# Kernel tuning notes

Hardware: AMD Instinct MI355X
Metric: run time of the kernel (lower is better)

## Reference

```python
import jax, jax.numpy as jnp
import numpy as np

N_NODES = 100000
N_EDGES = 1600000
EMB = 128
EDGE_DIMS = [6, 3]
BN_EPS = 1e-5


def setup_inputs() -> dict:
    key = jax.random.key(0)
    ks = jax.random.split(key, 16)
    inp = {
        "node_feats": jax.random.normal(ks[0], (N_NODES, EMB), jnp.float32),
        "edge_feat_0": jax.random.uniform(ks[1], (N_EDGES, EDGE_DIMS[0]), jnp.float32),
        "edge_feat_1": jax.random.uniform(ks[2], (N_EDGES, EDGE_DIMS[1]), jnp.float32),
        "src": jax.random.randint(ks[3], (N_EDGES,), 0, N_NODES, jnp.int32),
        "dst": jax.random.randint(ks[4], (N_EDGES,), 0, N_NODES, jnp.int32),
    }
    # edge embedding linears (MLP num_layers==1 -> plain Linear)
    s0 = 1.0 / np.sqrt(EDGE_DIMS[0])
    s1 = 1.0 / np.sqrt(EDGE_DIMS[1])
    inp["We0"] = jax.random.uniform(ks[5], (EDGE_DIMS[0], EMB), jnp.float32, -s0, s0)
    inp["be0"] = jax.random.uniform(ks[6], (EMB,), jnp.float32, -s0, s0)
    inp["We1"] = jax.random.uniform(ks[7], (EDGE_DIMS[1], EMB), jnp.float32, -s1, s1)
    inp["be1"] = jax.random.uniform(ks[8], (EMB,), jnp.float32, -s1, s1)
    # mlp: Linear(emb, 2*emb) -> ReLU -> Linear(2*emb, emb)
    sm = 1.0 / np.sqrt(EMB)
    sh = 1.0 / np.sqrt(2 * EMB)
    inp["W1"] = jax.random.uniform(ks[9], (EMB, 2 * EMB), jnp.float32, -sm, sm)
    inp["b1"] = jax.random.uniform(ks[10], (2 * EMB,), jnp.float32, -sm, sm)
    inp["W2"] = jax.random.uniform(ks[11], (2 * EMB, EMB), jnp.float32, -sh, sh)
    inp["b2"] = jax.random.uniform(ks[12], (EMB,), jnp.float32, -sh, sh)
    # batch norm affine params
    inp["gamma"] = jnp.ones((EMB,), jnp.float32)
    inp["beta"] = jnp.zeros((EMB,), jnp.float32)
    return inp


def reference(node_feats, edge_feat_0, edge_feat_1, src, dst,
              We0, be0, We1, be1, W1, b1, W2, b2, gamma, beta):
    n_nodes = node_feats.shape[0]
    # per-family edge embeddings, summed
    edge_embs = (edge_feat_0 @ We0 + be0) + (edge_feat_1 @ We1 + be1)  # [E, D]
    # u_add_e: gather src node feats, add edge emb
    msgs = node_feats[src] + edge_embs  # [E, D]
    # scatter-sum to destination nodes
    agg = jax.ops.segment_sum(msgs, dst, num_segments=n_nodes)  # [N, D]
    # MLP: Linear -> ReLU -> Linear
    h = jax.nn.relu(agg @ W1 + b1) @ W2 + b2  # [N, D]
    # BatchNorm1d (training mode: batch statistics, biased variance)
    mean = jnp.mean(h, axis=0)
    var = jnp.var(h, axis=0)
    h = (h - mean) * jax.lax.rsqrt(var + BN_EPS) * gamma + beta
    return h
```

## Files before the change

kernel.cpp:

```cpp
#include <hip/hip_runtime.h>

#define N_NODES 100000
#define N_EDGES 1600000
#define EMB 128
#define BM 16
#define NSLAB 64
#define BN_EPS 1e-5f

#define SCAN_BLK 512
#define NB_SCAN ((N_NODES + SCAN_BLK - 1) / SCAN_BLK)
#define NPAD (NB_SCAN * SCAN_BLK)

typedef short short8 __attribute__((ext_vector_type(8)));
typedef float floatx4 __attribute__((ext_vector_type(4)));

__device__ __forceinline__ ushort f2bf(float x) {
    unsigned u = __float_as_uint(x);
    u += 0x7fffu + ((u >> 16) & 1u);
    return (ushort)(u >> 16);
}
__device__ __forceinline__ float lo2f(unsigned p) {
    return __uint_as_float(p << 16);
}
__device__ __forceinline__ float hi2f(unsigned p) {
    return __uint_as_float(p & 0xffff0000u);
}

#define DPP_ADD(x, ctrl, mask) \
    ((x) + __int_as_float(__builtin_amdgcn_update_dpp(0, __float_as_int(x), ctrl, mask, 0xf, true)))

__device__ __forceinline__ float wave_sum63(float x) {
    x = DPP_ADD(x, 0x111, 0xf);
    x = DPP_ADD(x, 0x112, 0xf);
    x = DPP_ADD(x, 0x114, 0xf);
    x = DPP_ADD(x, 0x118, 0xf);
    x = DPP_ADD(x, 0x142, 0xa);
    x = DPP_ADD(x, 0x143, 0xc);
    return __int_as_float(__builtin_amdgcn_readlane(__float_as_int(x), 63));
}

__global__ __launch_bounds__(256) void setup_kernel(
    const float* __restrict__ nf, ushort* __restrict__ nfbf,
    const int* __restrict__ dst, int* __restrict__ counts,
    const float* __restrict__ W1, const float* __restrict__ W2,
    ushort* __restrict__ w1f, ushort* __restrict__ w2f)
{
    int gtid = blockIdx.x * 256 + threadIdx.x;
    long gstride = (long)gridDim.x * 256;

    if (gtid < 65536) {
        int idx = gtid;
        int i = idx & 7;
        int lane = (idx >> 3) & 63;
        int kloc = ((lane >> 4) << 3) + i;
        int nloc = lane & 15;
        if (idx < 32768) {
            int ks = (idx >> 9) & 3, nt = idx >> 11;
            w1f[idx] = f2bf(W1[(ks * 32 + kloc) * 256 + nt * 16 + nloc]);
        } else {
            int j = idx - 32768;
            int ks = (j >> 9) & 7, nt = j >> 12;
            w2f[j] = f2bf(W2[(ks * 32 + kloc) * 128 + nt * 16 + nloc]);
        }
    }

    long total = (long)N_NODES * EMB / 4;
    for (long p = gtid; p < total; p += gstride) {
        float4 v = ((const float4*)nf)[p];
        ushort4 o;
        o.x = f2bf(v.x); o.y = f2bf(v.y); o.z = f2bf(v.z); o.w = f2bf(v.w);
        ((ushort4*)nfbf)[p] = o;
    }

    for (long e = gtid; e < N_EDGES; e += gstride)
        atomicAdd(&counts[dst[e]], 1);
}

__global__ __launch_bounds__(SCAN_BLK) void scan_blocksum_kernel(
    const int* __restrict__ counts, int* __restrict__ blockSums)
{
    __shared__ int red[SCAN_BLK];
    int t = threadIdx.x;
    int i = blockIdx.x * SCAN_BLK + t;
    red[t] = (i < N_NODES) ? counts[i] : 0;
    __syncthreads();
    for (int s = SCAN_BLK / 2; s > 0; s >>= 1) {
        if (t < s) red[t] += red[t + s];
        __syncthreads();
    }
    if (t == 0) blockSums[blockIdx.x] = red[0];
}

__global__ __launch_bounds__(SCAN_BLK) void scan_final_kernel(
    const int* __restrict__ counts, const int* __restrict__ blockSums,
    int* __restrict__ offsets, int* __restrict__ cursor)
{
    __shared__ int s[SCAN_BLK];
    __shared__ int bs[256];
    int t = threadIdx.x;
    if (t < 256) bs[t] = (t < NB_SCAN) ? blockSums[t] : 0;
    __syncthreads();
    for (int off = 1; off < 256; off <<= 1) {
        int v = (t < 256 && t >= off) ? bs[t - off] : 0;
        __syncthreads();
        if (t < 256) bs[t] += v;
        __syncthreads();
    }
    int blockBase = (blockIdx.x == 0) ? 0 : bs[blockIdx.x - 1];

    int i = blockIdx.x * SCAN_BLK + t;
    int orig = (i < N_NODES) ? counts[i] : 0;
    s[t] = orig;
    __syncthreads();
    for (int off = 1; off < SCAN_BLK; off <<= 1) {
        int v = (t >= off) ? s[t - off] : 0;
        __syncthreads();
        s[t] += v;
        __syncthreads();
    }
    int excl = s[t] - orig + blockBase;
    if (i < N_NODES) { offsets[i] = excl; cursor[i] = excl; }
    if (i == N_NODES) offsets[N_NODES] = N_EDGES;
}

template<int RS>
__global__ __launch_bounds__(256) void scatter_kernel_t(
    const int* __restrict__ src, const int* __restrict__ dst,
    const float* __restrict__ ef0, const float* __restrict__ ef1,
    int* __restrict__ cursor, int* __restrict__ rec)
{
    int e = blockIdx.x * 256 + threadIdx.x;
    if (e >= N_EDGES) return;
    int t = dst[e];
    int pos = atomicAdd(&cursor[t], 1);

    const float2* p0 = (const float2*)(ef0 + (long)e * 6);
    float2 q0 = p0[0], q1 = p0[1], q2 = p0[2];
    const float* p1 = ef1 + (long)e * 3;
    float g0 = p1[0], g1 = p1[1], g2 = p1[2];

    int u0 = (int)((unsigned)f2bf(q0.x) | ((unsigned)f2bf(q0.y) << 16));
    int u1 = (int)((unsigned)f2bf(q1.x) | ((unsigned)f2bf(q1.y) << 16));
    int u2 = (int)((unsigned)f2bf(q2.x) | ((unsigned)f2bf(q2.y) << 16));
    int u3 = (int)((unsigned)f2bf(g0)   | ((unsigned)f2bf(g1) << 16));
    int u4 = (int)((unsigned)f2bf(g2));

    int* out = rec + (long)pos * RS;
    if constexpr (RS == 8) {
        ((int4*)out)[0] = make_int4(src[e], u0, u1, u2);
        ((int2*)out)[2] = make_int2(u3, u4);
    } else {
        ((int2*)out)[0] = make_int2(src[e], u0);
        ((int2*)out)[1] = make_int2(u1, u2);
        ((int2*)out)[2] = make_int2(u3, u4);
    }
}

template<int RS>
__device__ __forceinline__ int read_rec(const int* __restrict__ rec, long pos,
                                        float* fs) {
    const int* p = rec + pos * RS;
    int sid; unsigned w1, w2, w3, w4, w5;
    if constexpr (RS == 8) {
        int4 a = *(const int4*)p;
        int2 b = *(const int2*)(p + 4);
        sid = a.x; w1 = (unsigned)a.y; w2 = (unsigned)a.z; w3 = (unsigned)a.w;
        w4 = (unsigned)b.x; w5 = (unsigned)b.y;
    } else {
        int2 a = ((const int2*)p)[0], b = ((const int2*)p)[1], c = ((const int2*)p)[2];
        sid = a.x; w1 = (unsigned)a.y; w2 = (unsigned)b.x; w3 = (unsigned)b.y;
        w4 = (unsigned)c.x; w5 = (unsigned)c.y;
    }
    fs[0] += lo2f(w1); fs[1] += hi2f(w1);
    fs[2] += lo2f(w2); fs[3] += hi2f(w2);
    fs[4] += lo2f(w3); fs[5] += hi2f(w3);
    fs[6] += lo2f(w4); fs[7] += hi2f(w4);
    fs[8] += lo2f(w5);
    return sid;
}

template<int RS>
__device__ __forceinline__ void gather_full_chunks(
    int& base, int end, int lane, int q, int lp,
    const int* __restrict__ rec, const int4* __restrict__ nf16,
    float4& accA, float4& accB, float* fs)
{
    for (; base + 64 <= end; base += 64) {
        int sid = read_rec<RS>(rec, (long)(base + lane), fs);
#pragma unroll 4
        for (int j = 0; j < 16; ++j) {
            int s = __shfl(sid, 4 * j + q);
            int4 nv = nf16[(long)s * 16 + lp];
            accA.x += lo2f((unsigned)nv.x); accA.y += hi2f((unsigned)nv.x);
            accA.z += lo2f((unsigned)nv.y); accA.w += hi2f((unsigned)nv.y);
            accB.x += lo2f((unsigned)nv.z); accB.y += hi2f((unsigned)nv.z);
            accB.z += lo2f((unsigned)nv.w); accB.w += hi2f((unsigned)nv.w);
        }
    }
}

template<int RS>
__global__ __launch_bounds__(256, 8) void gather_kernel_t(
    const ushort* __restrict__ nfbf, const int* __restrict__ rec,
    const int* __restrict__ offsets,
    const float* __restrict__ We0, const float* __restrict__ be0,
    const float* __restrict__ We1, const float* __restrict__ be1,
    ushort* __restrict__ aggbf)
{
    int wv = threadIdx.x >> 6, lane = threadIdx.x & 63;
    int n0 = blockIdx.x * 8 + wv * 2;
    int q = lane >> 4, lp = lane & 15;
    const int4* nf16 = (const int4*)nfbf;

    int beg0 = offsets[n0];
    int mid  = offsets[n0 + 1];
    int end1 = offsets[n0 + 2];

    float4 a0A = make_float4(0.f, 0.f, 0.f, 0.f), a0B = a0A;
    float4 a1A = a0A, a1B = a0A;
    float fs0[9] = {}, fs1[9] = {};

    int b0 = beg0, b1 = mid;
    gather_full_chunks<RS>(b0, mid, lane, q, lp, rec, nf16, a0A, a0B, fs0);
    gather_full_chunks<RS>(b1, end1, lane, q, lp, rec, nf16, a1A, a1B, fs1);

    int m0 = mid - b0, m1 = end1 - b1;
    int sid0 = 0, sid1 = 0;
    if (lane < m0) sid0 = read_rec<RS>(rec, (long)(b0 + lane), fs0);
    if (lane < m1) sid1 = read_rec<RS>(rec, (long)(b1 + lane), fs1);

    int mx = m0 > m1 ? m0 : m1;
    int rounds = (mx + 3) >> 2;
#pragma unroll 4
    for (int j = 0; j < rounds; ++j) {
        int r = 4 * j + q;
        int s0 = __shfl(sid0, r);
        int s1 = __shfl(sid1, r);
        if (r < m0) {
            int4 nv = nf16[(long)s0 * 16 + lp];
            a0A.x += lo2f((unsigned)nv.x); a0A.y += hi2f((unsigned)nv.x);
            a0A.z += lo2f((unsigned)nv.y); a0A.w += hi2f((unsigned)nv.y);
            a0B.x += lo2f((unsigned)nv.z); a0B.y += hi2f((unsigned)nv.z);
            a0B.z += lo2f((unsigned)nv.w); a0B.w += hi2f((unsigned)nv.w);
        }
        if (r < m1) {
            int4 nv = nf16[(long)s1 * 16 + lp];
            a1A.x += lo2f((unsigned)nv.x); a1A.y += hi2f((unsigned)nv.x);
            a1A.z += lo2f((unsigned)nv.y); a1A.w += hi2f((unsigned)nv.y);
            a1B.x += lo2f((unsigned)nv.z); a1B.y += hi2f((unsigned)nv.z);
            a1B.z += lo2f((unsigned)nv.w); a1B.w += hi2f((unsigned)nv.w);
        }
    }

#define QRED(v) v += __shfl_xor(v, 16); v += __shfl_xor(v, 32);
    QRED(a0A.x) QRED(a0A.y) QRED(a0A.z) QRED(a0A.w)
    QRED(a0B.x) QRED(a0B.y) QRED(a0B.z) QRED(a0B.w)
    QRED(a1A.x) QRED(a1A.y) QRED(a1A.z) QRED(a1A.w)
    QRED(a1B.x) QRED(a1B.y) QRED(a1B.z) QRED(a1B.w)
#undef QRED

    float fk0[9], fk1[9];
#pragma unroll
    for (int k = 0; k < 9; ++k) {
        fk0[k] = wave_sum63(fs0[k]);
        fk1[k] = wave_sum63(fs1[k]);
    }

    int nodesel = q & 1;
    int hh = q >> 1;
    long myn = (long)n0 + nodesel;
    float deg = nodesel ? (float)(end1 - mid) : (float)(mid - beg0);
    float4 acc;
    {
        float4 selA, selB;
        selA.x = nodesel ? a1A.x : a0A.x; selA.y = nodesel ? a1A.y : a0A.y;
        selA.z = nodesel ? a1A.z : a0A.z; selA.w = nodesel ? a1A.w : a0A.w;
        selB.x = nodesel ? a1B.x : a0B.x; selB.y = nodesel ? a1B.y : a0B.y;
        selB.z = nodesel ? a1B.z : a0B.z; selB.w = nodesel ? a1B.w : a0B.w;
        acc.x = hh ? selB.x : selA.x; acc.y = hh ? selB.y : selA.y;
        acc.z = hh ? selB.z : selA.z; acc.w = hh ? selB.w : selA.w;
    }
    int fidx = 2 * lp + hh;
    float4 bb0 = ((const float4*)be0)[fidx];
    float4 bb1 = ((const float4*)be1)[fidx];
    float4 e;
    e.x = deg * (bb0.x + bb1.x); e.y = deg * (bb0.y + bb1.y);
    e.z = deg * (bb0.z + bb1.z); e.w = deg * (bb0.w + bb1.w);
#pragma unroll
    for (int k = 0; k < 6; ++k) {
        float f = nodesel ? fk1[k] : fk0[k];
        float4 w = ((const float4*)We0)[k * 32 + fidx];
        e.x = fmaf(f, w.x, e.x); e.y = fmaf(f, w.y, e.y);
        e.z = fmaf(f, w.z, e.z); e.w = fmaf(f, w.w, e.w);
    }
#pragma unroll
    for (int k = 0; k < 3; ++k) {
        float f = nodesel ? fk1[6 + k] : fk0[6 + k];
        float4 w = ((const float4*)We1)[k * 32 + fidx];
        e.x = fmaf(f, w.x, e.x); e.y = fmaf(f, w.y, e.y);
        e.z = fmaf(f, w.z, e.z); e.w = fmaf(f, w.w, e.w);
    }
    ushort4 o;
    o.x = f2bf(acc.x + e.x); o.y = f2bf(acc.y + e.y);
    o.z = f2bf(acc.z + e.z); o.w = f2bf(acc.w + e.w);
    ((ushort4*)aggbf)[myn * 32 + fidx] = o;
}

__global__ __launch_bounds__(256) void edge_scatter_kernel(
    const float* __restrict__ node_feats,
    const float* __restrict__ ef0,
    const float* __restrict__ ef1,
    const int* __restrict__ src,
    const int* __restrict__ dst,
    const float* __restrict__ We0, const float* __restrict__ be0,
    const float* __restrict__ We1, const float* __restrict__ be1,
    float* __restrict__ agg)
{
    __shared__ float wS[10 * EMB];
    int tid = threadIdx.x;
    for (int i = tid; i < 6 * EMB; i += 256) wS[i] = We0[i];
    for (int i = tid; i < 3 * EMB; i += 256) wS[6 * EMB + i] = We1[i];
    if (tid < EMB) wS[9 * EMB + tid] = be0[tid] + be1[tid];
    __syncthreads();

    int e = blockIdx.x * 2 + (tid >> 7);
    if (e >= N_EDGES) return;
    int d = tid & 127;
    int s = src[e];
    int t = dst[e];
    const float* f0 = ef0 + (long)e * 6;
    const float* f1 = ef1 + (long)e * 3;

    float emb = wS[9 * EMB + d];
#pragma unroll
    for (int k = 0; k < 6; ++k) emb = fmaf(f0[k], wS[k * EMB + d], emb);
#pragma unroll
    for (int k = 0; k < 3; ++k) emb = fmaf(f1[k], wS[6 * EMB + k * EMB + d], emb);

    float val = node_feats[(long)s * EMB + d] + emb;
    atomicAdd(&agg[(long)t * EMB + d], val);
}

__global__ __launch_bounds__(256) void mlp_mfma_kernel(
    const ushort* __restrict__ aggbf, ushort* __restrict__ hbf,
    const ushort* __restrict__ w1f, const ushort* __restrict__ w2f,
    const float* __restrict__ b1, const float* __restrict__ b2,
    float* __restrict__ stats)
{
    __shared__ __align__(16) char h1S[32 * 512];

    int tid = threadIdx.x;
    int lane = tid & 63;
    int wv = tid >> 6;
    long base = (long)blockIdx.x * 32;

    short8 a[2][4];
#pragma unroll
    for (int mt = 0; mt < 2; ++mt)
#pragma unroll
        for (int ks = 0; ks < 4; ++ks) {
            long row = base + mt * 16 + (lane & 15);
            a[mt][ks] = *(const short8*)&aggbf[row * EMB + ks * 32 + ((lane >> 4) << 3)];
        }

    floatx4 acc1[2][4];
#pragma unroll
    for (int nt = 0; nt < 4; ++nt) {
        float bias = b1[(wv * 4 + nt) * 16 + (lane & 15)];
#pragma unroll
        for (int mt = 0; mt < 2; ++mt)
            acc1[mt][nt] = (floatx4){bias, bias, bias, bias};
    }
#pragma unroll
    for (int ks = 0; ks < 4; ++ks) {
#pragma unroll
        for (int nt = 0; nt < 4; ++nt) {
            short8 b = *(const short8*)&w1f[(((wv * 4 + nt) * 4 + ks) * 64 + lane) * 8];
            acc1[0][nt] = __builtin_amdgcn_mfma_f32_16x16x32_bf16(a[0][ks], b, acc1[0][nt], 0, 0, 0);
            acc1[1][nt] = __builtin_amdgcn_mfma_f32_16x16x32_bf16(a[1][ks], b, acc1[1][nt], 0, 0, 0);
        }
    }
#pragma unroll
    for (int mt = 0; mt < 2; ++mt)
#pragma unroll
        for (int nt = 0; nt < 4; ++nt)
#pragma unroll
            for (int i = 0; i < 4; ++i) {
                int row = mt * 16 + ((lane >> 4) << 2) + i;
                int col = (wv * 4 + nt) * 16 + (lane & 15);
                float v = fmaxf(acc1[mt][nt][i], 0.f);
                *(ushort*)&h1S[row * 512 + ((2 * col) ^ ((row & 7) << 4))] = f2bf(v);
            }
    __syncthreads();

    int swz = (lane & 7) << 4;
    floatx4 acc2[2][2];
#pragma unroll
    for (int nt = 0; nt < 2; ++nt) {
        float bias = b2[(wv * 2 + nt) * 16 + (lane & 15)];
#pragma unroll
        for (int mt = 0; mt < 2; ++mt)
            acc2[mt][nt] = (floatx4){bias, bias, bias, bias};
    }
#pragma unroll
    for (int ks = 0; ks < 8; ++ks) {
        int kb = ks * 64 + ((lane >> 4) << 4);
        short8 a0 = *(const short8*)&h1S[(lane & 15) * 512 + (kb ^ swz)];
        short8 a1 = *(const short8*)&h1S[(16 + (lane & 15)) * 512 + (kb ^ swz)];
#pragma unroll
        for (int nt = 0; nt < 2; ++nt) {
            short8 b = *(const short8*)&w2f[(((wv * 2 + nt) * 8 + ks) * 64 + lane) * 8];
            acc2[0][nt] = __builtin_amdgcn_mfma_f32_16x16x32_bf16(a0, b, acc2[0][nt], 0, 0, 0);
            acc2[1][nt] = __builtin_amdgcn_mfma_f32_16x16x32_bf16(a1, b, acc2[1][nt], 0, 0, 0);
        }
    }

    float s[2] = {0.f, 0.f}, s2[2] = {0.f, 0.f};
#pragma unroll
    for (int nt = 0; nt < 2; ++nt) {
        int col = (wv * 2 + nt) * 16 + (lane & 15);
#pragma unroll
        for (int mt = 0; mt < 2; ++mt)
#pragma unroll
            for (int i = 0; i < 4; ++i) {
                int row = mt * 16 + ((lane >> 4) << 2) + i;
                float v = acc2[mt][nt][i];
                hbf[(base + row) * EMB + col] = f2bf(v);
                s[nt] += v;
                s2[nt] = fmaf(v, v, s2[nt]);
            }
    }
#pragma unroll
    for (int nt = 0; nt < 2; ++nt) {
        s[nt] += __shfl_xor(s[nt], 16);
        s[nt] += __shfl_xor(s[nt], 32);
        s2[nt] += __shfl_xor(s2[nt], 16);
        s2[nt] += __shfl_xor(s2[nt], 32);
    }
    if (lane < 16) {
        float* slab = stats + (blockIdx.x & (NSLAB - 1)) * (2 * EMB);
#pragma unroll
        for (int nt = 0; nt < 2; ++nt) {
            int col = (wv * 2 + nt) * 16 + lane;
            atomicAdd(&slab[col], s[nt]);
            atomicAdd(&slab[EMB + col], s2[nt]);
        }
    }
}

__global__ __launch_bounds__(256) void mlp_kernel(
    float* __restrict__ h,
    const float* __restrict__ W1, const float* __restrict__ b1,
    const float* __restrict__ W2, const float* __restrict__ b2,
    float* __restrict__ stats)
{
    __shared__ float aggS[BM][EMB];
    __shared__ float h1S[BM][2 * EMB];
    __shared__ float sredS[256];
    __shared__ float s2redS[256];

    int tid = threadIdx.x;
    long base = (long)blockIdx.x * BM;

    for (int i = tid; i < BM * EMB; i += 256)
        aggS[i >> 7][i & 127] = h[base * EMB + i];
    __syncthreads();

    {
        float acc[BM];
        float bias = b1[tid];
#pragma unroll
        for (int r = 0; r < BM; ++r) acc[r] = bias;
        for (int k = 0; k < EMB; ++k) {
            float w = W1[k * (2 * EMB) + tid];
#pragma unroll
            for (int r = 0; r < BM; ++r) acc[r] = fmaf(aggS[r][k], w, acc[r]);
        }
#pragma unroll
        for (int r = 0; r < BM; ++r) h1S[r][tid] = fmaxf(acc[r], 0.0f);
    }
    __syncthreads();

    {
        int c = tid & 127;
        int half = tid >> 7;
        float acc[8];
        float bias = b2[c];
#pragma unroll
        for (int r = 0; r < 8; ++r) acc[r] = bias;
        for (int k = 0; k < 2 * EMB; ++k) {
            float w = W2[k * EMB + c];
#pragma unroll
            for (int r = 0; r < 8; ++r) acc[r] = fmaf(h1S[half * 8 + r][k], w, acc[r]);
        }
        float s = 0.f, s2 = 0.f;
#pragma unroll
        for (int r = 0; r < 8; ++r) {
            h[(base + half * 8 + r) * EMB + c] = acc[r];
            s += acc[r];
            s2 = fmaf(acc[r], acc[r], s2);
        }
        sredS[tid] = s;
        s2redS[tid] = s2;
    }
    __syncthreads();
    if (tid < 128) {
        float s = sredS[tid] + sredS[tid + 128];
        float s2 = s2redS[tid] + s2redS[tid + 128];
        float* slab = stats + (blockIdx.x & (NSLAB - 1)) * (2 * EMB);
        atomicAdd(&slab[tid], s);
        atomicAdd(&slab[EMB + tid], s2);
    }
}

__global__ __launch_bounds__(256) void bn_apply_bf16_kernel(
    const ushort* __restrict__ hbf, float* __restrict__ out,
    const float* __restrict__ stats,
    const float* __restrict__ gamma, const float* __restrict__ beta)
{
    __shared__ float scS[EMB], shS[EMB];
    int tid = threadIdx.x;
    if (tid < EMB) {
        float s = 0.f, s2 = 0.f;
        for (int b = 0; b < NSLAB; ++b) {
            s += stats[b * (2 * EMB) + tid];
            s2 += stats[b * (2 * EMB) + EMB + tid];
        }
        float mean = s / (float)N_NODES;
        float var = s2 / (float)N_NODES - mean * mean;
        float sc = gamma[tid] * rsqrtf(var + BN_EPS);
        scS[tid] = sc;
        shS[tid] = beta[tid] - mean * sc;
    }
    __syncthreads();
    long total = (long)N_NODES * EMB / 8;
    long stride = (long)gridDim.x * blockDim.x;
    for (long p = (long)blockIdx.x * blockDim.x + threadIdx.x; p < total; p += stride) {
        uint4 v = ((const uint4*)hbf)[p];
        int c = (int)((p * 8) & 127);
        float4 o1, o2;
        o1.x = fmaf(lo2f(v.x), scS[c + 0], shS[c + 0]);
        o1.y = fmaf(hi2f(v.x), scS[c + 1], shS[c + 1]);
        o1.z = fmaf(lo2f(v.y), scS[c + 2], shS[c + 2]);
        o1.w = fmaf(hi2f(v.y), scS[c + 3], shS[c + 3]);
        o2.x = fmaf(lo2f(v.z), scS[c + 4], shS[c + 4]);
        o2.y = fmaf(hi2f(v.z), scS[c + 5], shS[c + 5]);
        o2.z = fmaf(lo2f(v.w), scS[c + 6], shS[c + 6]);
        o2.w = fmaf(hi2f(v.w), scS[c + 7], shS[c + 7]);
        ((float4*)out)[2 * p] = o1;
        ((float4*)out)[2 * p + 1] = o2;
    }
}

__global__ __launch_bounds__(256) void bn_apply_fused_kernel(
    float* __restrict__ h, const float* __restrict__ stats,
    const float* __restrict__ gamma, const float* __restrict__ beta)
{
    __shared__ float scS[EMB], shS[EMB];
    int tid = threadIdx.x;
    if (tid < EMB) {
        float s = 0.f, s2 = 0.f;
        for (int b = 0; b < NSLAB; ++b) {
            s += stats[b * (2 * EMB) + tid];
            s2 += stats[b * (2 * EMB) + EMB + tid];
        }
        float mean = s / (float)N_NODES;
        float var = s2 / (float)N_NODES - mean * mean;
        float sc = gamma[tid] * rsqrtf(var + BN_EPS);
        scS[tid] = sc;
        shS[tid] = beta[tid] - mean * sc;
    }
    __syncthreads();
    long total = (long)N_NODES * EMB / 4;
    long stride = (long)gridDim.x * blockDim.x;
    for (long i = (long)blockIdx.x * blockDim.x + threadIdx.x; i < total; i += stride) {
        float4 v = ((float4*)h)[i];
        int c = (int)((i * 4) & 127);
        v.x = fmaf(v.x, scS[c + 0], shS[c + 0]);
        v.y = fmaf(v.y, scS[c + 1], shS[c + 1]);
        v.z = fmaf(v.z, scS[c + 2], shS[c + 2]);
        v.w = fmaf(v.w, scS[c + 3], shS[c + 3]);
        ((float4*)h)[i] = v;
    }
}

extern "C" void kernel_launch(void* const* d_in, const int* in_sizes, int n_in,
                              void* d_out, int out_size, void* d_ws, size_t ws_size,
                              hipStream_t stream) {
    const float* node_feats = (const float*)d_in[0];
    const float* ef0 = (const float*)d_in[1];
    const float* ef1 = (const float*)d_in[2];
    const int* src = (const int*)d_in[3];
    const int* dst = (const int*)d_in[4];
    const float* We0 = (const float*)d_in[5];
    const float* be0 = (const float*)d_in[6];
    const float* We1 = (const float*)d_in[7];
    const float* be1 = (const float*)d_in[8];
    const float* W1 = (const float*)d_in[9];
    const float* b1 = (const float*)d_in[10];
    const float* W2 = (const float*)d_in[11];
    const float* b2 = (const float*)d_in[12];
    const float* gamma = (const float*)d_in[13];
    const float* beta = (const float*)d_in[14];

    float* out = (float*)d_out;
    ushort* aggbf = (ushort*)d_out;

    float* stats = (float*)d_ws;
    float* scaleshift = stats + NSLAB * 2 * EMB;
    int* counts = (int*)(scaleshift + 256);
    int* offsets = counts + NPAD;
    int* cursor = offsets + NPAD;
    int* blockSums = cursor + NPAD;
    ushort* w1f = (ushort*)(blockSums + 256);
    ushort* w2f = w1f + 32768;
    int* rec = (int*)(w2f + 32768);
    ushort* hbf = (ushort*)rec;

    ushort* nfbfA = (ushort*)(rec + (size_t)N_EDGES * 8);
    size_t needA = (size_t)((char*)(nfbfA + (size_t)N_NODES * EMB) - (char*)d_ws);
    ushort* nfbfB = (ushort*)(rec + (size_t)N_EDGES * 6);
    size_t needB = (size_t)((char*)(nfbfB + (size_t)N_NODES * EMB) - (char*)d_ws);

    if (ws_size >= needB) {
        bool tierA = (ws_size >= needA);
        ushort* nfbf = tierA ? nfbfA : nfbfB;

        hipMemsetAsync(d_ws, 0,
            (size_t)(NSLAB * 2 * EMB + 256) * sizeof(float) + (size_t)NPAD * sizeof(int),
            stream);
        setup_kernel<<<2048, 256, 0, stream>>>(
            node_feats, nfbf, dst, counts, W1, W2, w1f, w2f);
        scan_blocksum_kernel<<<NB_SCAN, SCAN_BLK, 0, stream>>>(counts, blockSums);
        scan_final_kernel<<<NB_SCAN, SCAN_BLK, 0, stream>>>(counts, blockSums, offsets, cursor);
        if (tierA) {
            scatter_kernel_t<8><<<(N_EDGES + 255) / 256, 256, 0, stream>>>(
                src, dst, ef0, ef1, cursor, rec);
            gather_kernel_t<8><<<N_NODES / 8, 256, 0, stream>>>(
                nfbf, rec, offsets, We0, be0, We1, be1, aggbf);
        } else {
            scatter_kernel_t<6><<<(N_EDGES + 255) / 256, 256, 0, stream>>>(
                src, dst, ef0, ef1, cursor, rec);
            gather_kernel_t<6><<<N_NODES / 8, 256, 0, stream>>>(
                nfbf, rec, offsets, We0, be0, We1, be1, aggbf);
        }
        mlp_mfma_kernel<<<N_NODES / 32, 256, 0, stream>>>(
            aggbf, hbf, w1f, w2f, b1, b2, stats);
        bn_apply_bf16_kernel<<<1024, 256, 0, stream>>>(hbf, out, stats, gamma, beta);
    } else {
        hipMemsetAsync(stats, 0, (size_t)NSLAB * 2 * EMB * sizeof(float), stream);
        hipMemsetAsync(d_out, 0, (size_t)N_NODES * EMB * sizeof(float), stream);
        edge_scatter_kernel<<<N_EDGES / 2, 256, 0, stream>>>(
            node_feats, ef0, ef1, src, dst, We0, be0, We1, be1, out);
        mlp_kernel<<<N_NODES / BM, 256, 0, stream>>>(out, W1, b1, W2, b2, stats);
        bn_apply_fused_kernel<<<4096, 256, 0, stream>>>(out, stats, gamma, beta);
    }
}
```

Before: 321.7 us.

## Split edge scatter into permutation pass and coalesced record build

The edge scatter now writes only a 4-byte edge index per sorted slot, so the atomic-ordered scattered writes are small. A second kernel walks the sorted positions, gathers the edge features and src ids through the permutation, and writes the 24-byte packed records contiguously. The record is also shrunk from the padded 32-byte layout to 24 bytes for the gather kernel. This adds an extra launch and random reads of the edge features, in exchange for coalesced record writes and less scattered traffic.

New measurement: 446.8 us. +38.9%, slower.

```diff
diff --git a/kernel.cpp b/kernel.cpp
--- a/kernel.cpp
+++ b/kernel.cpp
@@ -123,20 +123,27 @@
     if (i == N_NODES) offsets[N_NODES] = N_EDGES;
 }
 
-template<int RS>
-__global__ __launch_bounds__(256) void scatter_kernel_t(
-    const int* __restrict__ src, const int* __restrict__ dst,
-    const float* __restrict__ ef0, const float* __restrict__ ef1,
-    int* __restrict__ cursor, int* __restrict__ rec)
+__global__ __launch_bounds__(256) void scatter_perm_kernel(
+    const int* __restrict__ dst, int* __restrict__ cursor, int* __restrict__ perm)
 {
     int e = blockIdx.x * 256 + threadIdx.x;
     if (e >= N_EDGES) return;
-    int t = dst[e];
-    int pos = atomicAdd(&cursor[t], 1);
-
-    const float2* p0 = (const float2*)(ef0 + (long)e * 6);
+    int pos = atomicAdd(&cursor[dst[e]], 1);
+    perm[pos] = e;
+}
+
+__global__ __launch_bounds__(256) void build_rec_kernel(
+    const int* __restrict__ perm, const int* __restrict__ src,
+    const float* __restrict__ ef0, const float* __restrict__ ef1,
+    int* __restrict__ rec)
+{
+    int pos = blockIdx.x * 256 + threadIdx.x;
+    if (pos >= N_EDGES) return;
+    long e = perm[pos];
+
+    const float2* p0 = (const float2*)(ef0 + e * 6);
     float2 q0 = p0[0], q1 = p0[1], q2 = p0[2];
-    const float* p1 = ef1 + (long)e * 3;
+    const float* p1 = ef1 + e * 3;
     float g0 = p1[0], g1 = p1[1], g2 = p1[2];
 
     int u0 = (int)((unsigned)f2bf(q0.x) | ((unsigned)f2bf(q0.y) << 16));
@@ -145,48 +152,60 @@
     int u3 = (int)((unsigned)f2bf(g0)   | ((unsigned)f2bf(g1) << 16));
     int u4 = (int)((unsigned)f2bf(g2));
 
-    int* out = rec + (long)pos * RS;
-    if constexpr (RS == 8) {
-        ((int4*)out)[0] = make_int4(src[e], u0, u1, u2);
-        ((int2*)out)[2] = make_int2(u3, u4);
-    } else {
-        ((int2*)out)[0] = make_int2(src[e], u0);
-        ((int2*)out)[1] = make_int2(u1, u2);
-        ((int2*)out)[2] = make_int2(u3, u4);
-    }
-}
-
-template<int RS>
+    int2* out = (int2*)(rec + (long)pos * 6);
+    out[0] = make_int2(src[e], u0);
+    out[1] = make_int2(u1, u2);
+    out[2] = make_int2(u3, u4);
+}
+
+__global__ __launch_bounds__(256) void scatter24_kernel(
+    const int* __restrict__ src, const int* __restrict__ dst,
+    const float* __restrict__ ef0, const float* __restrict__ ef1,
+    int* __restrict__ cursor, int* __restrict__ rec)
+{
+    int e = blockIdx.x * 256 + threadIdx.x;
+    if (e >= N_EDGES) return;
+    int t = dst[e];
+    int pos = atomicAdd(&cursor[t], 1);
+
+    const float2* p0 = (const float2*)(ef0 + (long)e * 6);
+    float2 q0 = p0[0], q1 = p0[1], q2 = p0[2];
+    const float* p1 = ef1 + (long)e * 3;
+    float g0 = p1[0], g1 = p1[1], g2 = p1[2];
+
+    int u0 = (int)((unsigned)f2bf(q0.x) | ((unsigned)f2bf(q0.y) << 16));
+    int u1 = (int)((unsigned)f2bf(q1.x) | ((unsigned)f2bf(q1.y) << 16));
+    int u2 = (int)((unsigned)f2bf(q2.x) | ((unsigned)f2bf(q2.y) << 16));
+    int u3 = (int)((unsigned)f2bf(g0)   | ((unsigned)f2bf(g1) << 16));
+    int u4 = (int)((unsigned)f2bf(g2));
+
+    int2* out = (int2*)(rec + (long)pos * 6);
+    out[0] = make_int2(src[e], u0);
+    out[1] = make_int2(u1, u2);
+    out[2] = make_int2(u3, u4);
+}
+
 __device__ __forceinline__ int read_rec(const int* __restrict__ rec, long pos,
                                         float* fs) {
-    const int* p = rec + pos * RS;
-    int sid; unsigned w1, w2, w3, w4, w5;
-    if constexpr (RS == 8) {
-        int4 a = *(const int4*)p;
-        int2 b = *(const int2*)(p + 4);
-        sid = a.x; w1 = (unsigned)a.y; w2 = (unsigned)a.z; w3 = (unsigned)a.w;
-        w4 = (unsigned)b.x; w5 = (unsigned)b.y;
-    } else {
-        int2 a = ((const int2*)p)[0], b = ((const int2*)p)[1], c = ((const int2*)p)[2];
-        sid = a.x; w1 = (unsigned)a.y; w2 = (unsigned)b.x; w3 = (unsigned)b.y;
-        w4 = (unsigned)c.x; w5 = (unsigned)c.y;
-    }
+    const int* p = rec + pos * 6;
+    int2 a = ((const int2*)p)[0], b = ((const int2*)p)[1], c = ((const int2*)p)[2];
+    unsigned w1 = (unsigned)a.y, w2 = (unsigned)b.x, w3 = (unsigned)b.y;
+    unsigned w4 = (unsigned)c.x, w5 = (unsigned)c.y;
     fs[0] += lo2f(w1); fs[1] += hi2f(w1);
     fs[2] += lo2f(w2); fs[3] += hi2f(w2);
     fs[4] += lo2f(w3); fs[5] += hi2f(w3);
     fs[6] += lo2f(w4); fs[7] += hi2f(w4);
     fs[8] += lo2f(w5);
-    return sid;
-}
-
-template<int RS>
+    return a.x;
+}
+
 __device__ __forceinline__ void gather_full_chunks(
     int& base, int end, int lane, int q, int lp,
     const int* __restrict__ rec, const int4* __restrict__ nf16,
     float4& accA, float4& accB, float* fs)
 {
     for (; base + 64 <= end; base += 64) {
-        int sid = read_rec<RS>(rec, (long)(base + lane), fs);
+        int sid = read_rec(rec, (long)(base + lane), fs);
 #pragma unroll 4
         for (int j = 0; j < 16; ++j) {
             int s = __shfl(sid, 4 * j + q);
@@ -199,8 +218,7 @@
     }
 }
 
-template<int RS>
-__global__ __launch_bounds__(256, 8) void gather_kernel_t(
+__global__ __launch_bounds__(256, 8) void gather_kernel(
     const ushort* __restrict__ nfbf, const int* __restrict__ rec,
     const int* __restrict__ offsets,
     const float* __restrict__ We0, const float* __restrict__ be0,
@@ -221,13 +239,13 @@
     float fs0[9] = {}, fs1[9] = {};
 
     int b0 = beg0, b1 = mid;
-    gather_full_chunks<RS>(b0, mid, lane, q, lp, rec, nf16, a0A, a0B, fs0);
-    gather_full_chunks<RS>(b1, end1, lane, q, lp, rec, nf16, a1A, a1B, fs1);
+    gather_full_chunks(b0, mid, lane, q, lp, rec, nf16, a0A, a0B, fs0);
+    gather_full_chunks(b1, end1, lane, q, lp, rec, nf16, a1A, a1B, fs1);
 
     int m0 = mid - b0, m1 = end1 - b1;
     int sid0 = 0, sid1 = 0;
-    if (lane < m0) sid0 = read_rec<RS>(rec, (long)(b0 + lane), fs0);
-    if (lane < m1) sid1 = read_rec<RS>(rec, (long)(b1 + lane), fs1);
+    if (lane < m0) sid0 = read_rec(rec, (long)(b0 + lane), fs0);
+    if (lane < m1) sid1 = read_rec(rec, (long)(b1 + lane), fs1);
 
     int mx = m0 > m1 ? m0 : m1;
     int rounds = (mx + 3) >> 2;
@@ -614,17 +632,19 @@
     int* blockSums = cursor + NPAD;
     ushort* w1f = (ushort*)(blockSums + 256);
     ushort* w2f = w1f + 32768;
-    int* rec = (int*)(w2f + 32768);
-    ushort* hbf = (ushort*)rec;
-
-    ushort* nfbfA = (ushort*)(rec + (size_t)N_EDGES * 8);
+    int* perm = (int*)(w2f + 32768);
+    int* recA = perm + N_EDGES;
+    ushort* nfbfA = (ushort*)(recA + (size_t)N_EDGES * 6);
     size_t needA = (size_t)((char*)(nfbfA + (size_t)N_NODES * EMB) - (char*)d_ws);
-    ushort* nfbfB = (ushort*)(rec + (size_t)N_EDGES * 6);
+    int* recB = (int*)(w2f + 32768);
+    ushort* nfbfB = (ushort*)(recB + (size_t)N_EDGES * 6);
     size_t needB = (size_t)((char*)(nfbfB + (size_t)N_NODES * EMB) - (char*)d_ws);
 
     if (ws_size >= needB) {
         bool tierA = (ws_size >= needA);
+        int* rec = tierA ? recA : recB;
         ushort* nfbf = tierA ? nfbfA : nfbfB;
+        ushort* hbf = (ushort*)rec;
 
         hipMemsetAsync(d_ws, 0,
             (size_t)(NSLAB * 2 * EMB + 256) * sizeof(float) + (size_t)NPAD * sizeof(int),
@@ -634,16 +654,15 @@
         scan_blocksum_kernel<<<NB_SCAN, SCAN_BLK, 0, stream>>>(counts, blockSums);
         scan_final_kernel<<<NB_SCAN, SCAN_BLK, 0, stream>>>(counts, blockSums, offsets, cursor);
         if (tierA) {
-            scatter_kernel_t<8><<<(N_EDGES + 255) / 256, 256, 0, stream>>>(
+            scatter_perm_kernel<<<(N_EDGES + 255) / 256, 256, 0, stream>>>(dst, cursor, perm);
+            build_rec_kernel<<<(N_EDGES + 255) / 256, 256, 0, stream>>>(
+                perm, src, ef0, ef1, rec);
+        } else {
+            scatter24_kernel<<<(N_EDGES + 255) / 256, 256, 0, stream>>>(
                 src, dst, ef0, ef1, cursor, rec);
-            gather_kernel_t<8><<<N_NODES / 8, 256, 0, stream>>>(
-                nfbf, rec, offsets, We0, be0, We1, be1, aggbf);
-        } else {
-            scatter_kernel_t<6><<<(N_EDGES + 255) / 256, 256, 0, stream>>>(
-                src, dst, ef0, ef1, cursor, rec);
-            gather_kernel_t<6><<<N_NODES / 8, 256, 0, stream>>>(
-                nfbf, rec, offsets, We0, be0, We1, be1, aggbf);
-        }
+        }
+        gather_kernel<<<N_NODES / 8, 256, 0, stream>>>(
+            nfbf, rec, offsets, We0, be0, We1, be1, aggbf);
         mlp_mfma_kernel<<<N_NODES / 32, 256, 0, stream>>>(
             aggbf, hbf, w1f, w2f, b1, b2, stats);
         bn_apply_bf16_kernel<<<1024, 256, 0, stream>>>(hbf, out, stats, gamma, beta);
```
